# Optimization experiments

Hardware: AMD Instinct MI355X
Metric: run time of the kernel (lower is better)

The kernel has to match this reference:

```python
import jax, jax.numpy as jnp
import numpy as np
from jax import lax

C = 256  # out_channels
K2 = 1   # a_kernel_size // 2


def _alpha_weights():
    # generate_alpha_weights(dilation=1): (2, 3) constant
    s = float(np.sin(-np.pi / 4.0))
    c = float(np.cos(-np.pi / 4.0))
    aw = np.zeros((2, 3), dtype=np.float32)
    aw[0, 0] = c
    aw[1, 0] = -s
    aw[0, -1] = s
    aw[1, -1] = c
    return jnp.asarray(aw)


def setup_inputs() -> dict:
    key = jax.random.key(0)
    k1, k2, k3 = jax.random.split(key, 3)
    x = jax.random.normal(k1, (32, 256, 64, 64), dtype=jnp.float32)
    w = jax.random.normal(k2, (256, 256, 3, 3), dtype=jnp.float32) * 0.05
    alpha = jax.random.normal(k3, (C, K2, 2, 2), dtype=jnp.float32) * 0.5
    return {"x": x, "w": w, "alpha": alpha}


def _arma_forward(x, w, alpha):
    # moving-average: Conv2d 3x3, stride 1, zero padding 1, no bias
    y = lax.conv_general_dilated(
        x, w, window_strides=(1, 1), padding=[(1, 1), (1, 1)],
        dimension_numbers=("NCHW", "OIHW", "NCHW"))
    B, Co, H, W = y.shape

    aw = _alpha_weights()  # (2, 3)
    at = jnp.tanh(alpha)                       # (C, K2, 2, 2)
    A_xy = jnp.einsum('ckab,bj->ckaj', at, aw)  # (C, K2, 2, 3)
    A_xy = A_xy.at[:, :, :, 1].set(1.0)         # middle tap forced to 1
    A_x = A_xy[:, :, 0:1, :]                    # (C, K2, 1, 3)
    A_y = A_xy[:, :, 1:2, :]                    # (C, K2, 1, 3)
    A = jnp.einsum('ckai,ckbj->ckij', A_x, A_y)  # (C, K2, 3, 3) separable 2D filter
    # pad to (C, K2, H, W) then roll so the center tap sits at the origin
    A_pad = jnp.pad(A, ((0, 0), (0, 0), (0, H - 3), (0, W - 3)))
    A_roll = jnp.roll(A_pad, shift=(-1, -1), axis=(-2, -1))

    # circular AR recursion via frequency-domain division, per dilation chunk
    for k in range(K2):
        a = A_roll[:, k]                        # (C, H, W)
        Yf = jnp.fft.fft2(y) / jnp.fft.fft2(a)  # broadcast (B,C,H,W)/(C,H,W)
        y = jnp.real(jnp.fft.ifft2(Yf))
    return y


def reference(x, w, alpha):
    return _arma_forward(x, w, alpha)
```

## Files before the change

kernel.cpp:

```cpp
#include <hip/hip_runtime.h>
#include <cmath>
#include <stdint.h>

#define HH 64
#define WD 64
#define CIN 256
#define COUT 256
#define NB 32

typedef _Float16 half8 __attribute__((ext_vector_type(8)));
typedef _Float16 half4 __attribute__((ext_vector_type(4)));
typedef float floatx4 __attribute__((ext_vector_type(4)));
typedef float floatx16 __attribute__((ext_vector_type(16)));

#define SB() __builtin_amdgcn_sched_barrier(0)

__device__ __forceinline__ void glds16(const void* src, void* dst) {
    __builtin_amdgcn_global_load_lds((const __attribute__((address_space(1))) void*)src,
                                     (__attribute__((address_space(3))) void*)dst, 16, 0, 0);
}

__device__ __forceinline__ unsigned xmap(unsigned B) {
    return B + (B & 0xFFFFE000u);
}

__global__ __launch_bounds__(256) void prep_kernel(const float* __restrict__ x,
                                                   const float* __restrict__ w,
                                                   const float* __restrict__ alpha,
                                                   float* __restrict__ y,
                                                   _Float16* __restrict__ w16,
                                                   _Float16* __restrict__ gm,
                                                   float4* __restrict__ zp) {
    __shared__ _Float16 lt[32 * 72];
    __shared__ float gl[128];
    const int tid = threadIdx.x;
    const int bb = blockIdx.x;

    if (bb < 16384) {
        const int h = bb & 63;
        const int chunk = (bb >> 6) & 7;
        const int n = bb >> 9;
        {
            const int ci = tid >> 3;
            const int w8 = (tid & 7) * 8;
            const float* src = x + (((size_t)(n * 256 + chunk * 32 + ci) * 64 + h) * 64 + w8);
            const float4 a = *(const float4*)src;
            const float4 b = *(const float4*)(src + 4);
            half8 hv;
            hv[0] = (_Float16)a.x; hv[1] = (_Float16)a.y; hv[2] = (_Float16)a.z; hv[3] = (_Float16)a.w;
            hv[4] = (_Float16)b.x; hv[5] = (_Float16)b.y; hv[6] = (_Float16)b.z; hv[7] = (_Float16)b.w;
            *(half8*)&lt[ci * 72 + w8] = hv;
        }
        __syncthreads();
        {
            const int wq = tid >> 2;
            const int kc = tid & 3;
            half8 hv;
            #pragma unroll
            for (int j = 0; j < 8; ++j) hv[j] = lt[(kc * 8 + j) * 72 + wq];
            const unsigned L = ((((unsigned)(n * 8 + chunk) * 64 + h) * 64 + wq) * 32 + kc * 8);
            const unsigned M = xmap(L * 2u);
            *(half8*)((char*)y + M) = hv;
        }
    } else if (bb < 16384 + 2304) {
        const int idx = (bb - 16384) * 256 + tid;
        const int j = idx & 7;
        const int m = (idx >> 3) & 15;
        const int q = (idx >> 7) & 3;
        const int u = (idx >> 9) & 3;
        const int rest = idx >> 11;
        const int tap = rest % 9;
        const int rr = rest / 9;
        const int cb = rr & 3;
        const int chunk = rr >> 2;
        const int co = cb * 64 + u * 16 + m;
        const int ci = chunk * 32 + q * 8 + j;
        w16[idx] = (_Float16)w[(co * CIN + ci) * 9 + tap];
        if (bb == 16384) {
            float4 z; z.x = 0.f; z.y = 0.f; z.z = 0.f; z.w = 0.f;
            zp[tid] = z;
        }
    } else {
        const int c = bb - 18688;
        if (tid < 128) {
            const int r   = tid & 63;
            const int isv = tid >> 6;
            const float t0 = tanhf(alpha[c * 4 + isv * 2 + 0]);
            const float t1 = tanhf(alpha[c * 4 + isv * 2 + 1]);
            const float qq = 0.70710678118654752f;
            const float a0 = qq * (t0 + t1);
            const float a2 = qq * (t1 - t0);
            const float rev = 0.015625f;
            float ssum = 0.f;
            for (int p = 0; p < 64; ++p) {
                const float pr = (float)p * rev;
                const float re = 1.f + (a0 + a2) * __builtin_amdgcn_cosf(pr);
                const float im = (a0 - a2) * __builtin_amdgcn_sinf(pr);
                const float inv = 1.f / (re * re + im * im);
                const float ph = (float)((p * r) & 63) * rev;
                ssum += (__builtin_amdgcn_cosf(ph) * re + __builtin_amdgcn_sinf(ph) * im) * inv;
            }
            gl[tid] = ssum * (1.0f / 64.0f);
        }
        __syncthreads();
        #pragma unroll
        for (int it = 0; it < 4; ++it) {
            const int idx = it * 256 + tid;
            const int kc = idx & 7;
            const int row = (idx >> 3) & 63;
            const int which = idx >> 9;
            const float* g = gl + which * 64;
            half8 hv;
            #pragma unroll
            for (int j = 0; j < 8; ++j)
                hv[j] = (_Float16)g[(row - (kc * 8 + j)) & 63];
            *(half8*)&gm[((size_t)(c * 2 + which) * 64 + row) * 64 + ((kc ^ (row & 7)) * 8)] = hv;
        }
    }
}

__global__ __launch_bounds__(256, 2) void conv_mfma(const _Float16* __restrict__ w16,
                                                    const _Float16* __restrict__ zp,
                                                    float* __restrict__ y) {
    extern __shared__ __align__(16) _Float16 xs2[];
    const int tid  = threadIdx.x;
    const int lane = tid & 63;
    const int wv   = tid >> 6;
    const int m    = lane & 15;
    const int q    = lane >> 4;

    const int bid  = blockIdx.x;
    const int xcd  = bid & 7;
    const int idx  = bid >> 3;
    const int sub  = idx & 7;
    const int cb   = sub >> 1;
    const int wt   = sub & 1;
    const int pair = xcd * 16 + (idx >> 3);
    const int ht   = pair & 3;
    const int n    = pair >> 2;
    const int h0   = ht * 16;
    const int w0   = wt * 32;

    int soffB[10];
    #pragma unroll
    for (int it = 0; it < 10; ++it) {
        const int slot = it * 256 + tid;
        const int row  = (slot * 7711) >> 20;
        const int rem  = slot - row * 136;
        const int col  = rem >> 2;
        const int oct  = (rem & 3) ^ (col & 3);
        const int gh   = h0 - 1 + row;
        const int gw   = w0 - 1 + col;
        soffB[it] = ((unsigned)gh < 64u && (unsigned)gw < 64u)
                 ? (((gh * 64 + gw) * 32 + oct * 8) * 2) : -1;
    }

    int aoff[3];
    #pragma unroll
    for (int kx = 0; kx < 3; ++kx)
        aoff[kx] = (m + kx) * 32 + ((q ^ ((m + kx) & 3)) * 8);

    floatx4 acc[4][2][4];
    #pragma unroll
    for (int ro = 0; ro < 4; ++ro)
        #pragma unroll
        for (int cbk = 0; cbk < 2; ++cbk)
            #pragma unroll
            for (int u = 0; u < 4; ++u) acc[ro][cbk][u] = (floatx4)0.f;

    const char* yb = (const char*)y;

    {
        const unsigned cbb0 = (unsigned)n * 2097152u;
        #pragma unroll
        for (int it = 0; it < 10; ++it) {
            if (it * 256 + tid < 2448) {
                const void* src = (soffB[it] >= 0)
                    ? (const void*)(yb + xmap(cbb0 + (unsigned)soffB[it]))
                    : (const void*)(zp + (lane << 3));
                glds16(src, xs2 + (size_t)(it * 256 + wv * 64) * 8);
            }
        }
    }
    asm volatile("s_waitcnt vmcnt(0)" ::: "memory");
    __syncthreads();

    for (int c = 0; c < 8; ++c) {
        _Float16* bcur = xs2 + (c & 1) * 19584;
        _Float16* bnxt = xs2 + ((c & 1) ^ 1) * 19584;
        const _Float16* wchunk = w16 + (size_t)(c * 4 + cb) * 18432;
        const unsigned cbbn = (unsigned)(n * 8 + c + 1) * 262144u;
        const bool pf = (c < 7);

        #pragma unroll
        for (int kx = 0; kx < 3; ++kx) {
            half8 bf[3][4];
            #pragma unroll
            for (int ky = 0; ky < 3; ++ky)
                #pragma unroll
                for (int u = 0; u < 4; ++u)
                    bf[ky][u] = *(const half8*)&wchunk[(ky * 3 + kx) * 2048 + u * 512 + lane * 8];

            if (kx == 0 && pf) {
                SB();
                #pragma unroll
                for (int it = 0; it < 5; ++it) {
                    const void* src = (soffB[it] >= 0)
                        ? (const void*)(yb + xmap(cbbn + (unsigned)soffB[it]))
                        : (const void*)(zp + (lane << 3));
                    glds16(src, bnxt + (size_t)(it * 256 + wv * 64) * 8);
                }
                SB();
            }
            if (kx == 1 && pf) {
                SB();
                #pragma unroll
                for (int it = 5; it < 10; ++it) {
                    if (it * 256 + tid < 2448) {
                        const void* src = (soffB[it] >= 0)
                            ? (const void*)(yb + xmap(cbbn + (unsigned)soffB[it]))
                            : (const void*)(zp + (lane << 3));
                        glds16(src, bnxt + (size_t)(it * 256 + wv * 64) * 8);
                    }
                }
                SB();
            }

            #pragma unroll
            for (int cbk = 0; cbk < 2; ++cbk) {
                half8 af[6];
                #pragma unroll
                for (int rr = 0; rr < 6; ++rr)
                    af[rr] = *(const half8*)&bcur[(wv * 4 + rr) * 1088 + cbk * 512 + aoff[kx]];
                __builtin_amdgcn_s_setprio(1);
                #pragma unroll
                for (int ro = 0; ro < 4; ++ro)
                    #pragma unroll
                    for (int ky = 0; ky < 3; ++ky)
                        #pragma unroll
                        for (int u = 0; u < 4; ++u)
                            acc[ro][cbk][u] = __builtin_amdgcn_mfma_f32_16x16x32_f16(
                                bf[ky][u], af[ro + ky], acc[ro][cbk][u], 0, 0, 0);
                __builtin_amdgcn_s_setprio(0);
            }
        }
        asm volatile("s_waitcnt vmcnt(0)" ::: "memory");
        __syncthreads();
    }

    _Float16* y16o = (_Float16*)y;
    #pragma unroll
    for (int u = 0; u < 4; ++u) {
        #pragma unroll
        for (int r = 0; r < 4; ++r) {
            const int co = cb * 64 + u * 16 + q * 4 + r;
            _Float16* yp = y16o + (size_t)(n * COUT + co) * 8192 + 4096;
            #pragma unroll
            for (int ro = 0; ro < 4; ++ro)
                #pragma unroll
                for (int cbk = 0; cbk < 2; ++cbk)
                    yp[(h0 + wv * 4 + ro) * 64 + w0 + cbk * 16 + m] = (_Float16)acc[ro][cbk][u][r];
        }
    }
}

__global__ __launch_bounds__(256, 3) void solve_mfma(const _Float16* __restrict__ gm,
                                                     float* __restrict__ y) {
    __shared__ __align__(16) _Float16 Gsh[2 * 64 * 64];
    __shared__ __align__(16) _Float16 TT[4][64 * 64];
    const int tid  = threadIdx.x;
    const int lane = tid & 63;
    const int wv   = tid >> 6;
    const int l31  = lane & 31;
    const int kh   = lane >> 5;

    const int bid = blockIdx.x;
    const int wg  = (bid & 7) * 256 + (bid >> 3);
    const int c   = wg >> 3;
    const int nq  = wg & 7;
    const int n   = nq * 4 + wv;

    {
        const _Float16* gsrc = gm + (size_t)c * 8192;
        #pragma unroll
        for (int it = 0; it < 4; ++it)
            glds16(gsrc + (size_t)(it * 256 + tid) * 8, Gsh + (size_t)(it * 256 + wv * 64) * 8);
    }
    asm volatile("s_waitcnt vmcnt(0)" ::: "memory");
    __syncthreads();

    const _Float16* ysrc = (const _Float16*)y + ((size_t)n * 256 + c) * 8192 + 4096;
    float* yp = y + ((size_t)n * 256 + c) * 4096;
    _Float16* tt = TT[wv];

    floatx16 a1[2][2];
    #pragma unroll
    for (int tr = 0; tr < 2; ++tr)
        #pragma unroll
        for (int tc = 0; tc < 2; ++tc) a1[tr][tc] = (floatx16)0.f;

    half8 yf[2][4];
    #pragma unroll
    for (int tr = 0; tr < 2; ++tr)
        #pragma unroll
        for (int ks = 0; ks < 4; ++ks)
            yf[tr][ks] = *(const half8*)&ysrc[(32 * tr + l31) * 64 + ks * 16 + kh * 8];

    #pragma unroll
    for (int ks = 0; ks < 4; ++ks) {
        const int kc = ks * 2 + kh;
        half8 gv[2];
        #pragma unroll
        for (int tc = 0; tc < 2; ++tc) {
            const int row = 32 * tc + l31;
            gv[tc] = *(const half8*)&Gsh[4096 + row * 64 + ((kc ^ (row & 7)) * 8)];
        }
        #pragma unroll
        for (int tr = 0; tr < 2; ++tr)
            #pragma unroll
            for (int tc = 0; tc < 2; ++tc)
                a1[tr][tc] = __builtin_amdgcn_mfma_f32_32x32x16_f16(
                    yf[tr][ks], gv[tc], a1[tr][tc], 0, 0, 0);
    }

    #pragma unroll
    for (int tr = 0; tr < 2; ++tr) {
        #pragma unroll
        for (int tc = 0; tc < 2; ++tc) {
            const int tcol = 32 * tc + l31;
            #pragma unroll
            for (int q2 = 0; q2 < 4; ++q2) {
                half4 hv;
                #pragma unroll
                for (int rq = 0; rq < 4; ++rq) hv[rq] = (_Float16)a1[tr][tc][q2 * 4 + rq];
                *(half4*)&tt[tcol * 64 + (((4 * tr + q2) ^ (tcol & 7)) * 8) + 4 * kh] = hv;
            }
        }
    }
    asm volatile("s_waitcnt lgkmcnt(0)" ::: "memory");
    __builtin_amdgcn_sched_barrier(0);

    floatx16 a2[2][2];
    #pragma unroll
    for (int tr = 0; tr < 2; ++tr)
        #pragma unroll
        for (int tc = 0; tc < 2; ++tc) a2[tr][tc] = (floatx16)0.f;

    #pragma unroll
    for (int ks = 0; ks < 4; ++ks) {
        const int kc = ks * 2 + kh;
        half8 gu[2], tb[2];
        #pragma unroll
        for (int tr = 0; tr < 2; ++tr) {
            const int row = 32 * tr + l31;
            gu[tr] = *(const half8*)&Gsh[row * 64 + ((kc ^ (row & 7)) * 8)];
        }
        #pragma unroll
        for (int tc = 0; tc < 2; ++tc) {
            const int col = 32 * tc + l31;
            tb[tc] = *(const half8*)&tt[col * 64 + ((kc ^ (col & 7)) * 8)];
        }
        #pragma unroll
        for (int tr = 0; tr < 2; ++tr)
            #pragma unroll
            for (int tc = 0; tc < 2; ++tc)
                a2[tr][tc] = __builtin_amdgcn_mfma_f32_32x32x16_f16(
                    gu[tr], tb[tc], a2[tr][tc], 0, 0, 0);
    }

    #pragma unroll
    for (int tr = 0; tr < 2; ++tr)
        #pragma unroll
        for (int tc = 0; tc < 2; ++tc)
            #pragma unroll
            for (int reg = 0; reg < 16; ++reg) {
                const int row = 32 * tr + (reg & 3) + 8 * (reg >> 2) + 4 * kh;
                yp[row * 64 + 32 * tc + l31] = a2[tr][tc][reg];
            }
}

extern "C" void kernel_launch(void* const* d_in, const int* in_sizes, int n_in,
                              void* d_out, int out_size, void* d_ws, size_t ws_size,
                              hipStream_t stream) {
    const float* x     = (const float*)d_in[0];
    const float* w     = (const float*)d_in[1];
    const float* alpha = (const float*)d_in[2];
    float* y = (float*)d_out;

    _Float16* w16 = (_Float16*)d_ws;
    _Float16* gm  = (_Float16*)((char*)d_ws + 1179648);
    float4*   zp  = (float4*)((char*)d_ws + 5373952);

    static bool inited = false;
    if (!inited) {
        hipFuncSetAttribute((const void*)conv_mfma,
                            hipFuncAttributeMaxDynamicSharedMemorySize, 78336);
        inited = true;
    }

    prep_kernel  <<<dim3(18944), 256, 0, stream>>>(x, w, alpha, y, w16, gm, zp);
    conv_mfma    <<<dim3(1024),  256, 78336, stream>>>(w16, (const _Float16*)zp, y);
    solve_mfma   <<<dim3(2048),  256, 0, stream>>>(gm, y);
}
```

Measured before the change: 386.6 us.

## Split solve into two half-row passes to halve LDS scratch and raise occupancy

The frequency-domain solve kernel now runs its two-stage matrix product in two 32-row halves. The per-wave transposed scratch buffer is halved, which allows launch bounds of 4 blocks per CU instead of 3. The second half's y fragments are loaded while the first half computes, and the MFMA groups are wrapped in s_setprio. Separately, the prep kernel's x-to-fp16 transpose drops the LDS staging and reads strided global elements directly, giving up coalescing to save the LDS round trip and barrier.

New measurement: 382.3 us. Within noise of the previous version (-1.1%).

```diff
diff --git a/kernel.cpp b/kernel.cpp
--- a/kernel.cpp
+++ b/kernel.cpp
@@ -31,7 +31,6 @@
                                                    _Float16* __restrict__ w16,
                                                    _Float16* __restrict__ gm,
                                                    float4* __restrict__ zp) {
-    __shared__ _Float16 lt[32 * 72];
     __shared__ float gl[128];
     const int tid = threadIdx.x;
     const int bb = blockIdx.x;
@@ -40,28 +39,14 @@
         const int h = bb & 63;
         const int chunk = (bb >> 6) & 7;
         const int n = bb >> 9;
-        {
-            const int ci = tid >> 3;
-            const int w8 = (tid & 7) * 8;
-            const float* src = x + (((size_t)(n * 256 + chunk * 32 + ci) * 64 + h) * 64 + w8);
-            const float4 a = *(const float4*)src;
-            const float4 b = *(const float4*)(src + 4);
-            half8 hv;
-            hv[0] = (_Float16)a.x; hv[1] = (_Float16)a.y; hv[2] = (_Float16)a.z; hv[3] = (_Float16)a.w;
-            hv[4] = (_Float16)b.x; hv[5] = (_Float16)b.y; hv[6] = (_Float16)b.z; hv[7] = (_Float16)b.w;
-            *(half8*)&lt[ci * 72 + w8] = hv;
-        }
-        __syncthreads();
-        {
-            const int wq = tid >> 2;
-            const int kc = tid & 3;
-            half8 hv;
-            #pragma unroll
-            for (int j = 0; j < 8; ++j) hv[j] = lt[(kc * 8 + j) * 72 + wq];
-            const unsigned L = ((((unsigned)(n * 8 + chunk) * 64 + h) * 64 + wq) * 32 + kc * 8);
-            const unsigned M = xmap(L * 2u);
-            *(half8*)((char*)y + M) = hv;
-        }
+        const int kc = tid & 3;
+        const int wq = tid >> 2;
+        const float* src = x + (((size_t)(n * 256 + chunk * 32 + kc * 8) * 64 + h) * 64 + wq);
+        half8 hv;
+        #pragma unroll
+        for (int j = 0; j < 8; ++j) hv[j] = (_Float16)src[j * 4096];
+        const unsigned L = ((((unsigned)(n * 8 + chunk) * 64 + h) * 64 + wq) * 32 + kc * 8);
+        *(half8*)((char*)y + xmap(L * 2u)) = hv;
     } else if (bb < 16384 + 2304) {
         const int idx = (bb - 16384) * 256 + tid;
         const int j = idx & 7;
@@ -264,10 +249,10 @@
     }
 }
 
-__global__ __launch_bounds__(256, 3) void solve_mfma(const _Float16* __restrict__ gm,
+__global__ __launch_bounds__(256, 4) void solve_mfma(const _Float16* __restrict__ gm,
                                                      float* __restrict__ y) {
     __shared__ __align__(16) _Float16 Gsh[2 * 64 * 64];
-    __shared__ __align__(16) _Float16 TT[4][64 * 64];
+    __shared__ __align__(16) _Float16 TT[4][32 * 64];
     const int tid  = threadIdx.x;
     const int lane = tid & 63;
     const int wv   = tid >> 6;
@@ -286,86 +271,141 @@
         for (int it = 0; it < 4; ++it)
             glds16(gsrc + (size_t)(it * 256 + tid) * 8, Gsh + (size_t)(it * 256 + wv * 64) * 8);
     }
-    asm volatile("s_waitcnt vmcnt(0)" ::: "memory");
-    __syncthreads();
-
     const _Float16* ysrc = (const _Float16*)y + ((size_t)n * 256 + c) * 8192 + 4096;
     float* yp = y + ((size_t)n * 256 + c) * 4096;
     _Float16* tt = TT[wv];
 
-    floatx16 a1[2][2];
+    half8 yf0[4];
+    #pragma unroll
+    for (int ks = 0; ks < 4; ++ks)
+        yf0[ks] = *(const half8*)&ysrc[l31 * 64 + ks * 16 + kh * 8];
+
+    asm volatile("s_waitcnt vmcnt(0)" ::: "memory");
+    __syncthreads();
+
+    floatx16 a2[2][2];
     #pragma unroll
     for (int tr = 0; tr < 2; ++tr)
         #pragma unroll
-        for (int tc = 0; tc < 2; ++tc) a1[tr][tc] = (floatx16)0.f;
-
-    half8 yf[2][4];
-    #pragma unroll
-    for (int tr = 0; tr < 2; ++tr)
-        #pragma unroll
-        for (int ks = 0; ks < 4; ++ks)
-            yf[tr][ks] = *(const half8*)&ysrc[(32 * tr + l31) * 64 + ks * 16 + kh * 8];
-
-    #pragma unroll
-    for (int ks = 0; ks < 4; ++ks) {
-        const int kc = ks * 2 + kh;
-        half8 gv[2];
+        for (int tc = 0; tc < 2; ++tc) a2[tr][tc] = (floatx16)0.f;
+
+    {
+        floatx16 a1[2];
+        a1[0] = (floatx16)0.f; a1[1] = (floatx16)0.f;
+        #pragma unroll
+        for (int ks = 0; ks < 4; ++ks) {
+            const int kc = ks * 2 + kh;
+            half8 gv[2];
+            #pragma unroll
+            for (int tc = 0; tc < 2; ++tc) {
+                const int row = 32 * tc + l31;
+                gv[tc] = *(const half8*)&Gsh[4096 + row * 64 + ((kc ^ (row & 7)) * 8)];
+            }
+            __builtin_amdgcn_s_setprio(1);
+            #pragma unroll
+            for (int tc = 0; tc < 2; ++tc)
+                a1[tc] = __builtin_amdgcn_mfma_f32_32x32x16_f16(yf0[ks], gv[tc], a1[tc], 0, 0, 0);
+            __builtin_amdgcn_s_setprio(0);
+        }
         #pragma unroll
         for (int tc = 0; tc < 2; ++tc) {
-            const int row = 32 * tc + l31;
-            gv[tc] = *(const half8*)&Gsh[4096 + row * 64 + ((kc ^ (row & 7)) * 8)];
-        }
-        #pragma unroll
-        for (int tr = 0; tr < 2; ++tr)
-            #pragma unroll
-            for (int tc = 0; tc < 2; ++tc)
-                a1[tr][tc] = __builtin_amdgcn_mfma_f32_32x32x16_f16(
-                    yf[tr][ks], gv[tc], a1[tr][tc], 0, 0, 0);
-    }
-
-    #pragma unroll
-    for (int tr = 0; tr < 2; ++tr) {
-        #pragma unroll
-        for (int tc = 0; tc < 2; ++tc) {
-            const int tcol = 32 * tc + l31;
+            const int col = 32 * tc + l31;
             #pragma unroll
             for (int q2 = 0; q2 < 4; ++q2) {
                 half4 hv;
                 #pragma unroll
-                for (int rq = 0; rq < 4; ++rq) hv[rq] = (_Float16)a1[tr][tc][q2 * 4 + rq];
-                *(half4*)&tt[tcol * 64 + (((4 * tr + q2) ^ (tcol & 7)) * 8) + 4 * kh] = hv;
-            }
-        }
-    }
+                for (int rq = 0; rq < 4; ++rq) hv[rq] = (_Float16)a1[tc][q2 * 4 + rq];
+                *(half4*)&tt[col * 32 + ((q2 ^ (col & 3)) * 8) + 4 * kh] = hv;
+            }
+        }
+    }
+    half8 yf1[4];
+    #pragma unroll
+    for (int ks = 0; ks < 4; ++ks)
+        yf1[ks] = *(const half8*)&ysrc[(32 + l31) * 64 + ks * 16 + kh * 8];
+
     asm volatile("s_waitcnt lgkmcnt(0)" ::: "memory");
-    __builtin_amdgcn_sched_barrier(0);
-
-    floatx16 a2[2][2];
-    #pragma unroll
-    for (int tr = 0; tr < 2; ++tr)
-        #pragma unroll
-        for (int tc = 0; tc < 2; ++tc) a2[tr][tc] = (floatx16)0.f;
-
-    #pragma unroll
-    for (int ks = 0; ks < 4; ++ks) {
-        const int kc = ks * 2 + kh;
+    SB();
+    #pragma unroll
+    for (int ks2 = 0; ks2 < 2; ++ks2) {
+        const int kc2 = ks2 * 2 + kh;
         half8 gu[2], tb[2];
         #pragma unroll
         for (int tr = 0; tr < 2; ++tr) {
             const int row = 32 * tr + l31;
-            gu[tr] = *(const half8*)&Gsh[row * 64 + ((kc ^ (row & 7)) * 8)];
+            gu[tr] = *(const half8*)&Gsh[row * 64 + ((kc2 ^ (row & 7)) * 8)];
         }
         #pragma unroll
         for (int tc = 0; tc < 2; ++tc) {
             const int col = 32 * tc + l31;
-            tb[tc] = *(const half8*)&tt[col * 64 + ((kc ^ (col & 7)) * 8)];
-        }
+            tb[tc] = *(const half8*)&tt[col * 32 + ((kc2 ^ (col & 3)) * 8)];
+        }
+        __builtin_amdgcn_s_setprio(1);
         #pragma unroll
         for (int tr = 0; tr < 2; ++tr)
             #pragma unroll
             for (int tc = 0; tc < 2; ++tc)
-                a2[tr][tc] = __builtin_amdgcn_mfma_f32_32x32x16_f16(
-                    gu[tr], tb[tc], a2[tr][tc], 0, 0, 0);
+                a2[tr][tc] = __builtin_amdgcn_mfma_f32_32x32x16_f16(gu[tr], tb[tc], a2[tr][tc], 0, 0, 0);
+        __builtin_amdgcn_s_setprio(0);
+    }
+
+    {
+        floatx16 a1[2];
+        a1[0] = (floatx16)0.f; a1[1] = (floatx16)0.f;
+        asm volatile("s_waitcnt vmcnt(0)" ::: "memory");
+        #pragma unroll
+        for (int ks = 0; ks < 4; ++ks) {
+            const int kc = ks * 2 + kh;
+            half8 gv[2];
+            #pragma unroll
+            for (int tc = 0; tc < 2; ++tc) {
+                const int row = 32 * tc + l31;
+                gv[tc] = *(const half8*)&Gsh[4096 + row * 64 + ((kc ^ (row & 7)) * 8)];
+            }
+            __builtin_amdgcn_s_setprio(1);
+            #pragma unroll
+            for (int tc = 0; tc < 2; ++tc)
+                a1[tc] = __builtin_amdgcn_mfma_f32_32x32x16_f16(yf1[ks], gv[tc], a1[tc], 0, 0, 0);
+            __builtin_amdgcn_s_setprio(0);
+        }
+        asm volatile("s_waitcnt lgkmcnt(0)" ::: "memory");
+        SB();
+        #pragma unroll
+        for (int tc = 0; tc < 2; ++tc) {
+            const int col = 32 * tc + l31;
+            #pragma unroll
+            for (int q2 = 0; q2 < 4; ++q2) {
+                half4 hv;
+                #pragma unroll
+                for (int rq = 0; rq < 4; ++rq) hv[rq] = (_Float16)a1[tc][q2 * 4 + rq];
+                *(half4*)&tt[col * 32 + ((q2 ^ (col & 3)) * 8) + 4 * kh] = hv;
+            }
+        }
+    }
+    asm volatile("s_waitcnt lgkmcnt(0)" ::: "memory");
+    SB();
+    #pragma unroll
+    for (int ks2 = 0; ks2 < 2; ++ks2) {
+        const int kc2 = ks2 * 2 + kh;
+        const int gkc = 4 + kc2;
+        half8 gu[2], tb[2];
+        #pragma unroll
+        for (int tr = 0; tr < 2; ++tr) {
+            const int row = 32 * tr + l31;
+            gu[tr] = *(const half8*)&Gsh[row * 64 + ((gkc ^ (row & 7)) * 8)];
+        }
+        #pragma unroll
+        for (int tc = 0; tc < 2; ++tc) {
+            const int col = 32 * tc + l31;
+            tb[tc] = *(const half8*)&tt[col * 32 + ((kc2 ^ (col & 3)) * 8)];
+        }
+        __builtin_amdgcn_s_setprio(1);
+        #pragma unroll
+        for (int tr = 0; tr < 2; ++tr)
+            #pragma unroll
+            for (int tc = 0; tc < 2; ++tc)
+                a2[tr][tc] = __builtin_amdgcn_mfma_f32_32x32x16_f16(gu[tr], tb[tc], a2[tr][tc], 0, 0, 0);
+        __builtin_amdgcn_s_setprio(0);
     }
 
     #pragma unroll
```
